# Performance work log

Measured on AMD Instinct MI355X. Metric: run time of the kernel, lower is better.

## Reference

```python
import jax, jax.numpy as jnp
import numpy as np

NUM_BANDS = 64
LATENT = 256
HIDDEN = 512
G = 8
K = 1024
GD = LATENT // G  # 32
BETA = 0.25


def setup_inputs() -> dict:
    key = jax.random.key(0)
    ks = jax.random.split(key, 10)
    B, T = 16, 1000
    bands = jax.random.normal(ks[0], (B, T, NUM_BANDS), dtype=jnp.float32)
    s = 0.02
    enc_w1 = jax.random.normal(ks[1], (NUM_BANDS, HIDDEN), dtype=jnp.float32) * s
    enc_b1 = jnp.zeros((HIDDEN,), dtype=jnp.float32)
    enc_w2 = jax.random.normal(ks[2], (HIDDEN, LATENT), dtype=jnp.float32) * s
    enc_b2 = jnp.zeros((LATENT,), dtype=jnp.float32)
    codebooks = jax.random.normal(ks[3], (G, K, GD), dtype=jnp.float32) * 0.1
    dec_w1 = jax.random.normal(ks[4], (LATENT, HIDDEN), dtype=jnp.float32) * s
    dec_b1 = jnp.zeros((HIDDEN,), dtype=jnp.float32)
    dec_w2 = jax.random.normal(ks[5], (HIDDEN, NUM_BANDS), dtype=jnp.float32) * s
    dec_b2 = jnp.zeros((NUM_BANDS,), dtype=jnp.float32)
    return {
        "bands": bands,
        "enc_w1": enc_w1, "enc_b1": enc_b1, "enc_w2": enc_w2, "enc_b2": enc_b2,
        "codebooks": codebooks,
        "dec_w1": dec_w1, "dec_b1": dec_b1, "dec_w2": dec_w2, "dec_b2": dec_b2,
    }


def _mlp(x, w1, b1, w2, b2):
    # TimeDistributedMLP: Linear -> ReLU -> Linear applied on last dim
    return jax.nn.relu(x @ w1 + b1) @ w2 + b2


def reference(bands, enc_w1, enc_b1, enc_w2, enc_b2, codebooks,
              dec_w1, dec_b1, dec_w2, dec_b2):
    B, T, _ = bands.shape
    z_e = _mlp(bands, enc_w1, enc_b1, enc_w2, enc_b2)  # (B,T,LATENT)

    # Grouped VQ over flattened frames
    parts = z_e.reshape(B * T, G, GD)                   # (N,G,gd)
    zn = jnp.sum(parts * parts, axis=-1)[:, :, None]    # (N,G,1)
    cn = jnp.sum(codebooks * codebooks, axis=-1)[None]  # (1,G,K)
    cross = jnp.einsum('ngd,gkd->ngk', parts, codebooks)
    dist = zn - 2.0 * cross + cn                        # (N,G,K)
    idx = jnp.argmin(dist, axis=-1)                     # (N,G) int
    z_q = codebooks[jnp.arange(G)[None, :], idx]        # (N,G,gd) gather

    # straight-through estimator
    z_q_st = parts + jax.lax.stop_gradient(z_q - parts)

    # per-group mean losses, summed over groups
    codebook_loss = jnp.sum(jnp.mean((jax.lax.stop_gradient(z_q) - parts) ** 2, axis=(0, 2)))
    commit_loss = jnp.sum(jnp.mean((z_q - jax.lax.stop_gradient(parts)) ** 2, axis=(0, 2)))
    vq_loss = BETA * (codebook_loss + commit_loss)  # epoch=None -> beta_eff = beta

    z_q_out = z_q_st.reshape(B, T, LATENT)
    idx_out = idx.reshape(B, T, G)
    bands_hat = _mlp(z_q_out, dec_w1, dec_b1, dec_w2, dec_b2)
    return (bands_hat, z_e, z_q_out, idx_out, vq_loss)
```

## Files before the change

kernel.cpp:

```cpp
#include <hip/hip_runtime.h>

#define NBANDS 64
#define LATENT 256
#define HIDDEN 512
#define GQ 8
#define KQ 1024
#define GD 32
#define NROWS 16000

#define OUT_BH   0
#define OUT_ZE   1024000
#define OUT_ZQ   5120000
#define OUT_IDX  9216000
#define OUT_LOSS 9344000

#define WS_H     0
#define WS_H2BF_F  0
#define WS_ZQB_F   4096000
#define WS_W1B_F   6144000
#define WS_W2B_F   6209536
#define WS_CBH_F   6240000
#define WS_CBM_F   6400000
#define WS_CBL_F   6560000
#define WS_CN    8192000
#define WS_LOSS  8200192

typedef __attribute__((ext_vector_type(8))) short bf16x8;
typedef __attribute__((ext_vector_type(4))) float f32x4;

__device__ __forceinline__ unsigned short f2bf(float f) {
  unsigned u = __builtin_bit_cast(unsigned, f);
  unsigned r = u + 0x7FFFu + ((u >> 16) & 1u);
  return (unsigned short)(r >> 16);
}

__device__ __forceinline__ float bf2f(unsigned short h) {
  return __builtin_bit_cast(float, ((unsigned)h) << 16);
}

__device__ __forceinline__ void split3(float x, unsigned short& h,
                                       unsigned short& m, unsigned short& l) {
  h = f2bf(x);
  const float r1 = x - bf2f(h);
  m = f2bf(r1);
  const float r2 = r1 - bf2f(m);
  l = f2bf(r2);
}

template<int BN, int TM, int TN, int BK, bool RELU>
__global__ __launch_bounds__(256) void gemm_f32(
    const float* __restrict__ A, const float* __restrict__ B,
    const float* __restrict__ bias, float* __restrict__ C,
    int M, int N, int K) {
  constexpr int BM = 128;
  constexpr int NTX = BN / TN;
  constexpr int AF4 = BK / 8;
  constexpr int QPR = BN / 4;
  constexpr int BF4 = BK * BN / 1024;

  __shared__ float As[BK][BM + 8];
  __shared__ float Bs[BK][BN + 4];

  const int tid = threadIdx.x;
  const int tx = tid % NTX;
  const int ty = tid / NTX;
  const int row0 = blockIdx.y * BM;
  const int col0 = blockIdx.x * BN;

  const int arow = tid >> 1;
  const int akq  = (tid & 1) * (BK / 2);

  float acc[TM][TN] = {};

  for (int k0 = 0; k0 < K; k0 += BK) {
    float4 av[AF4], bv[BF4];
#pragma unroll
    for (int q = 0; q < AF4; ++q)
      av[q] = *reinterpret_cast<const float4*>(
          &A[(size_t)(row0 + arow) * K + k0 + akq + q * 4]);
#pragma unroll
    for (int t = 0; t < BF4; ++t) {
      const int qq = tid * BF4 + t;
      const int bk = qq / QPR, bn4 = qq % QPR;
      bv[t] = *reinterpret_cast<const float4*>(
          &B[(size_t)(k0 + bk) * N + col0 + bn4 * 4]);
    }
    __syncthreads();
#pragma unroll
    for (int q = 0; q < AF4; ++q) {
      As[akq + q * 4 + 0][arow] = av[q].x;
      As[akq + q * 4 + 1][arow] = av[q].y;
      As[akq + q * 4 + 2][arow] = av[q].z;
      As[akq + q * 4 + 3][arow] = av[q].w;
    }
#pragma unroll
    for (int t = 0; t < BF4; ++t) {
      const int qq = tid * BF4 + t;
      const int bk = qq / QPR, bn4 = qq % QPR;
      *reinterpret_cast<float4*>(&Bs[bk][bn4 * 4]) = bv[t];
    }
    __syncthreads();

#pragma unroll
    for (int kk = 0; kk < BK; ++kk) {
      float a[TM], b[TN];
#pragma unroll
      for (int q = 0; q < TM / 4; ++q) {
        float4 v = *reinterpret_cast<const float4*>(&As[kk][ty * TM + q * 4]);
        a[q * 4 + 0] = v.x; a[q * 4 + 1] = v.y;
        a[q * 4 + 2] = v.z; a[q * 4 + 3] = v.w;
      }
#pragma unroll
      for (int q = 0; q < TN / 4; ++q) {
        float4 v = *reinterpret_cast<const float4*>(&Bs[kk][tx * TN + q * 4]);
        b[q * 4 + 0] = v.x; b[q * 4 + 1] = v.y;
        b[q * 4 + 2] = v.z; b[q * 4 + 3] = v.w;
      }
#pragma unroll
      for (int i = 0; i < TM; ++i)
#pragma unroll
        for (int j = 0; j < TN; ++j)
          acc[i][j] = fmaf(a[i], b[j], acc[i][j]);
    }
  }

  float bb[TN];
#pragma unroll
  for (int q = 0; q < TN / 4; ++q) {
    float4 v = *reinterpret_cast<const float4*>(&bias[col0 + tx * TN + q * 4]);
    bb[q * 4 + 0] = v.x; bb[q * 4 + 1] = v.y;
    bb[q * 4 + 2] = v.z; bb[q * 4 + 3] = v.w;
  }
#pragma unroll
  for (int i = 0; i < TM; ++i) {
    const int r = row0 + ty * TM + i;
#pragma unroll
    for (int q = 0; q < TN / 4; ++q) {
      float4 v;
      float* vp = &v.x;
#pragma unroll
      for (int j = 0; j < 4; ++j) {
        float t = acc[i][q * 4 + j] + bb[q * 4 + j];
        if (RELU) t = fmaxf(t, 0.0f);
        vp[j] = t;
      }
      *reinterpret_cast<float4*>(&C[(size_t)r * N + col0 + tx * TN + q * 4]) = v;
    }
  }
}

template<int WM, bool OUT_BF16, bool DO_LOSS>
__global__ __launch_bounds__(256) void gemm_bf16_mfma(
    const unsigned short* __restrict__ A, const unsigned short* __restrict__ BT,
    const float* __restrict__ bias, void* __restrict__ Cout,
    int M, int N, int K,
    const float* __restrict__ loss_acc, float* __restrict__ loss_out) {
  constexpr int BM = 4 * WM;
  constexpr int MT = WM / 16;

  __shared__ unsigned short As[BM][40];
  __shared__ unsigned short Bs[64][40];

  const int tid  = threadIdx.x;
  const int wave = tid >> 6;
  const int lane = tid & 63;
  const int quad = lane >> 4;
  const int l16  = lane & 15;
  const int row0 = blockIdx.y * BM;
  const int col0 = blockIdx.x * 64;

  if (DO_LOSS && blockIdx.x == 0 && blockIdx.y == 0 && tid == 0)
    loss_out[0] = 0.5f * loss_acc[0] / (float)((size_t)NROWS * GD);

  f32x4 acc[MT][4];
#pragma unroll
  for (int mt = 0; mt < MT; ++mt)
#pragma unroll
    for (int nt = 0; nt < 4; ++nt) acc[mt][nt] = (f32x4){0.f, 0.f, 0.f, 0.f};

  for (int k0 = 0; k0 < K; k0 += 32) {
    __syncthreads();
    if constexpr (BM == 128) {
      const int r = tid >> 1, seg = (tid & 1) * 16;
      const uint4* src = reinterpret_cast<const uint4*>(
          &A[(size_t)(row0 + r) * K + k0 + seg]);
      uint4* dst = reinterpret_cast<uint4*>(&As[r][seg]);
      dst[0] = src[0]; dst[1] = src[1];
    } else {
      const int r = tid >> 2, seg = (tid & 3) * 8;
      *reinterpret_cast<uint4*>(&As[r][seg]) =
          *reinterpret_cast<const uint4*>(&A[(size_t)(row0 + r) * K + k0 + seg]);
    }
    {
      const int n = tid >> 2, kc = (tid & 3) * 8;
      *reinterpret_cast<uint4*>(&Bs[n][kc]) =
          *reinterpret_cast<const uint4*>(&BT[(size_t)(col0 + n) * K + k0 + kc]);
    }
    __syncthreads();

    bf16x8 af[MT], bf[4];
#pragma unroll
    for (int mt = 0; mt < MT; ++mt)
      af[mt] = *reinterpret_cast<const bf16x8*>(
          &As[wave * WM + mt * 16 + l16][quad * 8]);
#pragma unroll
    for (int nt = 0; nt < 4; ++nt)
      bf[nt] = *reinterpret_cast<const bf16x8*>(&Bs[nt * 16 + l16][quad * 8]);
#pragma unroll
    for (int mt = 0; mt < MT; ++mt)
#pragma unroll
      for (int nt = 0; nt < 4; ++nt)
        acc[mt][nt] = __builtin_amdgcn_mfma_f32_16x16x32_bf16(
            af[mt], bf[nt], acc[mt][nt], 0, 0, 0);
  }

#pragma unroll
  for (int mt = 0; mt < MT; ++mt)
#pragma unroll
    for (int nt = 0; nt < 4; ++nt) {
      const int col = col0 + nt * 16 + l16;
      const float bv = bias[col];
#pragma unroll
      for (int r = 0; r < 4; ++r) {
        const int grow = row0 + wave * WM + mt * 16 + quad * 4 + r;
        float v = acc[mt][nt][r] + bv;
        if constexpr (OUT_BF16) {
          v = fmaxf(v, 0.0f);
          ((unsigned short*)Cout)[(size_t)grow * N + col] = f2bf(v);
        } else {
          ((float*)Cout)[(size_t)grow * N + col] = v;
        }
      }
    }
}

__global__ void prep_cn(const float* __restrict__ cb, float* __restrict__ cn,
                        float* __restrict__ loss_acc) {
  const int i = blockIdx.x * 256 + threadIdx.x;
  if (i == 0) loss_acc[0] = 0.0f;
  if (i < GQ * KQ) {
    const float* c = cb + (size_t)i * GD;
    float s = 0.0f;
#pragma unroll
    for (int d = 0; d < GD; ++d) s = fmaf(c[d], c[d], s);
    cn[i] = -0.5f * s;
  }
}

__global__ void prep_wT(const float* __restrict__ w1, const float* __restrict__ w2,
                        const float* __restrict__ cbk,
                        unsigned short* __restrict__ w1bT,
                        unsigned short* __restrict__ w2bT,
                        unsigned short* __restrict__ cbh,
                        unsigned short* __restrict__ cbm,
                        unsigned short* __restrict__ cbl) {
  const int t = blockIdx.x * 256 + threadIdx.x;
  if (t < 16384) {
    const int n = t >> 5, k0 = (t & 31) * 8;
    alignas(16) unsigned short o[8];
#pragma unroll
    for (int q = 0; q < 8; ++q) o[q] = f2bf(w1[(size_t)(k0 + q) * HIDDEN + n]);
    *reinterpret_cast<uint4*>(&w1bT[(size_t)n * LATENT + k0]) =
        *reinterpret_cast<const uint4*>(o);
  } else if (t < 20480) {
    const int u = t - 16384;
    const int n = u >> 6, k0 = (u & 63) * 8;
    alignas(16) unsigned short o[8];
#pragma unroll
    for (int q = 0; q < 8; ++q) o[q] = f2bf(w2[(size_t)(k0 + q) * NBANDS + n]);
    *reinterpret_cast<uint4*>(&w2bT[(size_t)n * HIDDEN + k0]) =
        *reinterpret_cast<const uint4*>(o);
  } else if (t < 53248) {
    const int e0 = (t - 20480) * 8;
    alignas(16) unsigned short oh[8], om[8], ol[8];
#pragma unroll
    for (int q = 0; q < 8; ++q) split3(cbk[e0 + q], oh[q], om[q], ol[q]);
    *reinterpret_cast<uint4*>(&cbh[e0]) = *reinterpret_cast<const uint4*>(oh);
    *reinterpret_cast<uint4*>(&cbm[e0]) = *reinterpret_cast<const uint4*>(om);
    *reinterpret_cast<uint4*>(&cbl[e0]) = *reinterpret_cast<const uint4*>(ol);
  }
}

struct VqStg { uint4 h, m, l; float c; };

__device__ __forceinline__ void vq_ldg(
    VqStg& s, const unsigned short* __restrict__ cbh,
    const unsigned short* __restrict__ cbm,
    const unsigned short* __restrict__ cbl,
    const float* __restrict__ cng, int gsh, int ch, int tid) {
  const int o = gsh + ch * 2048 + tid * 8;
  s.h = *reinterpret_cast<const uint4*>(&cbh[o]);
  s.m = *reinterpret_cast<const uint4*>(&cbm[o]);
  s.l = *reinterpret_cast<const uint4*>(&cbl[o]);
  if (tid < 64) s.c = cng[ch * 64 + tid];
}

__device__ __forceinline__ void vq_stl(
    unsigned short (&buf)[6272], const VqStg& s, int tid) {
  *reinterpret_cast<uint4*>(&buf[tid * 8])        = s.h;
  *reinterpret_cast<uint4*>(&buf[2048 + tid * 8]) = s.m;
  *reinterpret_cast<uint4*>(&buf[4096 + tid * 8]) = s.l;
  if (tid < 64) *reinterpret_cast<float*>(&buf[6144 + tid * 2]) = s.c;
}

__device__ __forceinline__ void vq_pair(
    const bf16x8 (&ah)[2], const bf16x8 (&am)[2], const bf16x8 (&al)[2],
    const unsigned short (&buf)[6272], int laneoff, int nt0, int ch, int l16,
    float (&best)[8], int (&bidx)[8]) {
  bf16x8 Fh[2], Fm[2], Fl[2];
  float  Fc[2];
#pragma unroll
  for (int p = 0; p < 2; ++p) {
    const int off = laneoff + (nt0 + p) * 512;
    Fh[p] = *reinterpret_cast<const bf16x8*>(&buf[off]);
    Fm[p] = *reinterpret_cast<const bf16x8*>(&buf[2048 + off]);
    Fl[p] = *reinterpret_cast<const bf16x8*>(&buf[4096 + off]);
    Fc[p] = *reinterpret_cast<const float*>(&buf[6144 + (((nt0 + p) * 16 + l16) << 1)]);
  }
  f32x4 a00 = {Fc[0], Fc[0], Fc[0], Fc[0]};
  f32x4 a01 = a00;
  f32x4 a10 = {Fc[1], Fc[1], Fc[1], Fc[1]};
  f32x4 a11 = a10;
  a00 = __builtin_amdgcn_mfma_f32_16x16x32_bf16(ah[0], Fh[0], a00, 0, 0, 0);
  a01 = __builtin_amdgcn_mfma_f32_16x16x32_bf16(ah[1], Fh[0], a01, 0, 0, 0);
  a10 = __builtin_amdgcn_mfma_f32_16x16x32_bf16(ah[0], Fh[1], a10, 0, 0, 0);
  a11 = __builtin_amdgcn_mfma_f32_16x16x32_bf16(ah[1], Fh[1], a11, 0, 0, 0);
  a00 = __builtin_amdgcn_mfma_f32_16x16x32_bf16(ah[0], Fm[0], a00, 0, 0, 0);
  a01 = __builtin_amdgcn_mfma_f32_16x16x32_bf16(ah[1], Fm[0], a01, 0, 0, 0);
  a10 = __builtin_amdgcn_mfma_f32_16x16x32_bf16(ah[0], Fm[1], a10, 0, 0, 0);
  a11 = __builtin_amdgcn_mfma_f32_16x16x32_bf16(ah[1], Fm[1], a11, 0, 0, 0);
  a00 = __builtin_amdgcn_mfma_f32_16x16x32_bf16(am[0], Fh[0], a00, 0, 0, 0);
  a01 = __builtin_amdgcn_mfma_f32_16x16x32_bf16(am[1], Fh[0], a01, 0, 0, 0);
  a10 = __builtin_amdgcn_mfma_f32_16x16x32_bf16(am[0], Fh[1], a10, 0, 0, 0);
  a11 = __builtin_amdgcn_mfma_f32_16x16x32_bf16(am[1], Fh[1], a11, 0, 0, 0);
  a00 = __builtin_amdgcn_mfma_f32_16x16x32_bf16(ah[0], Fl[0], a00, 0, 0, 0);
  a01 = __builtin_amdgcn_mfma_f32_16x16x32_bf16(ah[1], Fl[0], a01, 0, 0, 0);
  a10 = __builtin_amdgcn_mfma_f32_16x16x32_bf16(ah[0], Fl[1], a10, 0, 0, 0);
  a11 = __builtin_amdgcn_mfma_f32_16x16x32_bf16(ah[1], Fl[1], a11, 0, 0, 0);
  a00 = __builtin_amdgcn_mfma_f32_16x16x32_bf16(am[0], Fm[0], a00, 0, 0, 0);
  a01 = __builtin_amdgcn_mfma_f32_16x16x32_bf16(am[1], Fm[0], a01, 0, 0, 0);
  a10 = __builtin_amdgcn_mfma_f32_16x16x32_bf16(am[0], Fm[1], a10, 0, 0, 0);
  a11 = __builtin_amdgcn_mfma_f32_16x16x32_bf16(am[1], Fm[1], a11, 0, 0, 0);
  a00 = __builtin_amdgcn_mfma_f32_16x16x32_bf16(al[0], Fh[0], a00, 0, 0, 0);
  a01 = __builtin_amdgcn_mfma_f32_16x16x32_bf16(al[1], Fh[0], a01, 0, 0, 0);
  a10 = __builtin_amdgcn_mfma_f32_16x16x32_bf16(al[0], Fh[1], a10, 0, 0, 0);
  a11 = __builtin_amdgcn_mfma_f32_16x16x32_bf16(al[1], Fh[1], a11, 0, 0, 0);
  {
    const int code = ch * 64 + nt0 * 16 + l16;
#pragma unroll
    for (int r = 0; r < 4; ++r) {
      if (a00[r] > best[r])     { best[r]     = a00[r]; bidx[r]     = code; }
      if (a01[r] > best[4 + r]) { best[4 + r] = a01[r]; bidx[4 + r] = code; }
    }
  }
  {
    const int code = ch * 64 + (nt0 + 1) * 16 + l16;
#pragma unroll
    for (int r = 0; r < 4; ++r) {
      if (a10[r] > best[r])     { best[r]     = a10[r]; bidx[r]     = code; }
      if (a11[r] > best[4 + r]) { best[4 + r] = a11[r]; bidx[4 + r] = code; }
    }
  }
}

__global__ __launch_bounds__(256, 3) void vq_mfma(
    const float* __restrict__ z_e, const float* __restrict__ cb,
    const float* __restrict__ cnh,
    const unsigned short* __restrict__ cbh,
    const unsigned short* __restrict__ cbm,
    const unsigned short* __restrict__ cbl,
    float* __restrict__ z_q, unsigned short* __restrict__ zqb,
    float* __restrict__ idx_out, float* __restrict__ loss_acc) {
  __shared__ __align__(16) unsigned short lds[2][6272];

  const int g    = blockIdx.y;
  const int row0 = blockIdx.x * 128;
  const int tid  = threadIdx.x;
  const int wave = tid >> 6;
  const int lane = tid & 63;
  const int quad = lane >> 4;
  const int l16  = lane & 15;

  const int gsh = g * (KQ * GD);
  const float* cng = cnh + g * KQ;
  const size_t cb0 = (size_t)g * KQ * GD;
  const int laneoff = l16 * 32 + quad * 8;

  VqStg sX, sY;
  vq_ldg(sX, cbh, cbm, cbl, cng, gsh, 0, tid);

  bf16x8 ah[2], am[2], al[2];
#pragma unroll
  for (int mt = 0; mt < 2; ++mt) {
    const float* zp = &z_e[(size_t)(row0 + wave * 32 + mt * 16 + l16) * LATENT
                           + g * GD + quad * 8];
    const float4 x0 = *reinterpret_cast<const float4*>(zp);
    const float4 x1 = *reinterpret_cast<const float4*>(zp + 4);
    const float xv[8] = {x0.x, x0.y, x0.z, x0.w, x1.x, x1.y, x1.z, x1.w};
    bf16x8 vh, vm, vl;
#pragma unroll
    for (int j = 0; j < 8; ++j) {
      unsigned short sh, sm, sl;
      split3(xv[j], sh, sm, sl);
      vh[j] = (short)sh; vm[j] = (short)sm; vl[j] = (short)sl;
    }
    ah[mt] = vh; am[mt] = vm; al[mt] = vl;
  }

  float best[8];
  int   bidx[8];
#pragma unroll
  for (int i = 0; i < 8; ++i) { best[i] = -3.0e38f; bidx[i] = 0; }

  vq_stl(lds[0], sX, tid);
  vq_ldg(sY, cbh, cbm, cbl, cng, gsh, 1, tid);
  __syncthreads();

#pragma unroll 1
  for (int cp = 0; cp < 8; ++cp) {
    const int ch = 2 * cp;
    if (ch < 14) vq_ldg(sX, cbh, cbm, cbl, cng, gsh, ch + 2, tid);
    vq_pair(ah, am, al, lds[0], laneoff, 0, ch, l16, best, bidx);
    vq_pair(ah, am, al, lds[0], laneoff, 2, ch, l16, best, bidx);
    vq_stl(lds[1], sY, tid);
    __syncthreads();

    const int ch2 = ch + 1;
    if (ch2 < 14) vq_ldg(sY, cbh, cbm, cbl, cng, gsh, ch2 + 2, tid);
    vq_pair(ah, am, al, lds[1], laneoff, 0, ch2, l16, best, bidx);
    vq_pair(ah, am, al, lds[1], laneoff, 2, ch2, l16, best, bidx);
    if (ch2 < 15) {
      vq_stl(lds[0], sX, tid);
      __syncthreads();
    }
  }

  float sse_local = 0.0f;
#pragma unroll
  for (int s8 = 0; s8 < 8; ++s8) {
    float mb = best[s8];
    int   mi = bidx[s8];
#pragma unroll
    for (int m = 1; m < 16; m <<= 1) {
      const float ov = __shfl_xor(mb, m, 64);
      const int   oi = __shfl_xor(mi, m, 64);
      if (ov > mb || (ov == mb && oi < mi)) { mb = ov; mi = oi; }
    }
    const int mt  = s8 >> 2;
    const int r   = s8 & 3;
    const int row = row0 + wave * 32 + mt * 16 + quad * 4 + r;
    const float2 cw = *reinterpret_cast<const float2*>(
        &cb[cb0 + (size_t)mi * GD + 2 * l16]);
    const float2 zv = *reinterpret_cast<const float2*>(
        &z_e[(size_t)row * LATENT + g * GD + 2 * l16]);
    const float d0 = cw.x - zv.x;
    const float d1 = cw.y - zv.y;
    sse_local = fmaf(d0, d0, fmaf(d1, d1, sse_local));
    *reinterpret_cast<float2*>(
        &z_q[(size_t)row * LATENT + g * GD + 2 * l16]) = cw;
    const unsigned pz = (unsigned)f2bf(cw.x) | ((unsigned)f2bf(cw.y) << 16);
    *reinterpret_cast<unsigned*>(
        &zqb[(size_t)row * LATENT + g * GD + 2 * l16]) = pz;
    if (l16 == 0) idx_out[(size_t)row * GQ + g] = (float)mi;
  }

#pragma unroll
  for (int m = 1; m < 64; m <<= 1) sse_local += __shfl_xor(sse_local, m, 64);
  if (lane == 0) atomicAdd(loss_acc, sse_local);
}

extern "C" void kernel_launch(void* const* d_in, const int* in_sizes, int n_in,
                              void* d_out, int out_size, void* d_ws, size_t ws_size,
                              hipStream_t stream) {
  const float* bands  = (const float*)d_in[0];
  const float* enc_w1 = (const float*)d_in[1];
  const float* enc_b1 = (const float*)d_in[2];
  const float* enc_w2 = (const float*)d_in[3];
  const float* enc_b2 = (const float*)d_in[4];
  const float* cbooks = (const float*)d_in[5];
  const float* dec_w1 = (const float*)d_in[6];
  const float* dec_b1 = (const float*)d_in[7];
  const float* dec_w2 = (const float*)d_in[8];
  const float* dec_b2 = (const float*)d_in[9];

  float* out = (float*)d_out;
  float* ws  = (float*)d_ws;

  float* bands_hat = out + OUT_BH;
  float* z_e       = out + OUT_ZE;
  float* z_q       = out + OUT_ZQ;
  float* idx_f     = out + OUT_IDX;
  float* loss_out  = out + OUT_LOSS;

  float* H        = ws + WS_H;
  float* cn       = ws + WS_CN;
  float* loss_acc = ws + WS_LOSS;
  unsigned short* h2bf = (unsigned short*)(ws + WS_H2BF_F);
  unsigned short* zqb  = (unsigned short*)(ws + WS_ZQB_F);
  unsigned short* w1bT = (unsigned short*)(ws + WS_W1B_F);
  unsigned short* w2bT = (unsigned short*)(ws + WS_W2B_F);
  unsigned short* cbh  = (unsigned short*)(ws + WS_CBH_F);
  unsigned short* cbm  = (unsigned short*)(ws + WS_CBM_F);
  unsigned short* cbl  = (unsigned short*)(ws + WS_CBL_F);

  prep_cn<<<dim3(32), dim3(256), 0, stream>>>(cbooks, cn, loss_acc);

  gemm_f32<128, 8, 8, 16, true ><<<dim3(HIDDEN / 128, NROWS / 128), dim3(256), 0, stream>>>(
      bands, enc_w1, enc_b1, H, NROWS, HIDDEN, NBANDS);
  gemm_f32<64, 4, 8, 32, false><<<dim3(LATENT / 64, NROWS / 128), dim3(256), 0, stream>>>(
      H, enc_w2, enc_b2, z_e, NROWS, LATENT, HIDDEN);

  prep_wT<<<dim3(208), dim3(256), 0, stream>>>(
      dec_w1, dec_w2, cbooks, w1bT, w2bT, cbh, cbm, cbl);

  vq_mfma<<<dim3(NROWS / 128, GQ), dim3(256), 0, stream>>>(
      z_e, cbooks, cn, cbh, cbm, cbl, z_q, zqb, idx_f, loss_acc);

  gemm_bf16_mfma<32, true, true ><<<dim3(HIDDEN / 64, NROWS / 128), dim3(256), 0, stream>>>(
      zqb, w1bT, dec_b1, (void*)h2bf, NROWS, HIDDEN, LATENT, loss_acc, loss_out);
  gemm_bf16_mfma<16, false, false><<<dim3(NBANDS / 64, NROWS / 64), dim3(256), 0, stream>>>(
      h2bf, w2bT, dec_b2, (void*)bands_hat, NROWS, NBANDS, HIDDEN, loss_acc, loss_out);
}
```

Measured before the change: 320.0 us.

## Pre-swizzle codebook chunks into LDS-ready records and halve VQ staging registers

The prep kernel now writes the hi/mid/lo bf16 codebook splits and the norm terms into per-chunk records already laid out in MFMA fragment order. The VQ kernel can then copy each record into LDS contiguously and read fragments with lane-linear offsets, which should avoid strided LDS reads and bank conflicts. Staging uses one register set instead of two, and launch bounds are raised to 4 blocks per CU to reduce register pressure and raise occupancy. In exchange the prep kernel does a scattered write pattern and runs more threads to copy the norms into the records.

```diff
diff --git a/kernel.cpp b/kernel.cpp
--- a/kernel.cpp
+++ b/kernel.cpp
@@ -19,9 +19,8 @@
 #define WS_ZQB_F   4096000
 #define WS_W1B_F   6144000
 #define WS_W2B_F   6209536
-#define WS_CBH_F   6240000
-#define WS_CBM_F   6400000
-#define WS_CBL_F   6560000
+#define WS_REC_F   6240000
+#define VQ_REC_SH  6272
 #define WS_CN    8192000
 #define WS_LOSS  8200192
 
@@ -248,12 +247,10 @@
 }
 
 __global__ void prep_wT(const float* __restrict__ w1, const float* __restrict__ w2,
-                        const float* __restrict__ cbk,
+                        const float* __restrict__ cbk, const float* __restrict__ cn,
                         unsigned short* __restrict__ w1bT,
                         unsigned short* __restrict__ w2bT,
-                        unsigned short* __restrict__ cbh,
-                        unsigned short* __restrict__ cbm,
-                        unsigned short* __restrict__ cbl) {
+                        unsigned short* __restrict__ rec) {
   const int t = blockIdx.x * 256 + threadIdx.x;
   if (t < 16384) {
     const int n = t >> 5, k0 = (t & 31) * 8;
@@ -272,46 +269,53 @@
         *reinterpret_cast<const uint4*>(o);
   } else if (t < 53248) {
     const int e0 = (t - 20480) * 8;
+    const int gidx = e0 >> 15;
+    const int w    = e0 & 32767;
+    const int code = w >> 5;
+    const int d0   = w & 31;
+    const int quad = d0 >> 3;
+    const int ch   = code >> 6;
+    const int cw   = code & 63;
+    const int nt   = cw >> 4;
+    const int l16  = cw & 15;
+    const int slot = nt * 64 + quad * 16 + l16;
+    unsigned short* recb = rec + (size_t)(gidx * 16 + ch) * VQ_REC_SH;
     alignas(16) unsigned short oh[8], om[8], ol[8];
 #pragma unroll
     for (int q = 0; q < 8; ++q) split3(cbk[e0 + q], oh[q], om[q], ol[q]);
-    *reinterpret_cast<uint4*>(&cbh[e0]) = *reinterpret_cast<const uint4*>(oh);
-    *reinterpret_cast<uint4*>(&cbm[e0]) = *reinterpret_cast<const uint4*>(om);
-    *reinterpret_cast<uint4*>(&cbl[e0]) = *reinterpret_cast<const uint4*>(ol);
-  }
-}
-
-struct VqStg { uint4 h, m, l; float c; };
-
-__device__ __forceinline__ void vq_ldg(
-    VqStg& s, const unsigned short* __restrict__ cbh,
-    const unsigned short* __restrict__ cbm,
-    const unsigned short* __restrict__ cbl,
-    const float* __restrict__ cng, int gsh, int ch, int tid) {
-  const int o = gsh + ch * 2048 + tid * 8;
-  s.h = *reinterpret_cast<const uint4*>(&cbh[o]);
-  s.m = *reinterpret_cast<const uint4*>(&cbm[o]);
-  s.l = *reinterpret_cast<const uint4*>(&cbl[o]);
-  if (tid < 64) s.c = cng[ch * 64 + tid];
-}
-
-__device__ __forceinline__ void vq_stl(
-    unsigned short (&buf)[6272], const VqStg& s, int tid) {
-  *reinterpret_cast<uint4*>(&buf[tid * 8])        = s.h;
-  *reinterpret_cast<uint4*>(&buf[2048 + tid * 8]) = s.m;
-  *reinterpret_cast<uint4*>(&buf[4096 + tid * 8]) = s.l;
-  if (tid < 64) *reinterpret_cast<float*>(&buf[6144 + tid * 2]) = s.c;
+    *reinterpret_cast<uint4*>(&recb[slot * 8]) =
+        *reinterpret_cast<const uint4*>(oh);
+    *reinterpret_cast<uint4*>(&recb[2048 + slot * 8]) =
+        *reinterpret_cast<const uint4*>(om);
+    *reinterpret_cast<uint4*>(&recb[4096 + slot * 8]) =
+        *reinterpret_cast<const uint4*>(ol);
+  } else if (t < 61440) {
+    const int i = t - 53248;
+    const int gidx = i >> 10, code = i & 1023;
+    const int ch = code >> 6, cw = code & 63;
+    unsigned short* recb = rec + (size_t)(gidx * 16 + ch) * VQ_REC_SH;
+    *reinterpret_cast<float*>(&recb[6144 + cw * 2]) = cn[(size_t)gidx * KQ + code];
+  }
+}
+
+__device__ __forceinline__ void vq_write(
+    unsigned short (&buf)[VQ_REC_SH], int tid,
+    const uint4& h, const uint4& m, const uint4& l, float c) {
+  *reinterpret_cast<uint4*>(&buf[tid * 8])        = h;
+  *reinterpret_cast<uint4*>(&buf[2048 + tid * 8]) = m;
+  *reinterpret_cast<uint4*>(&buf[4096 + tid * 8]) = l;
+  if (tid < 64) *reinterpret_cast<float*>(&buf[6144 + tid * 2]) = c;
 }
 
 __device__ __forceinline__ void vq_pair(
     const bf16x8 (&ah)[2], const bf16x8 (&am)[2], const bf16x8 (&al)[2],
-    const unsigned short (&buf)[6272], int laneoff, int nt0, int ch, int l16,
+    const unsigned short (&buf)[VQ_REC_SH], int lane, int l16, int nt0, int ch,
     float (&best)[8], int (&bidx)[8]) {
   bf16x8 Fh[2], Fm[2], Fl[2];
   float  Fc[2];
 #pragma unroll
   for (int p = 0; p < 2; ++p) {
-    const int off = laneoff + (nt0 + p) * 512;
+    const int off = ((nt0 + p) * 64 + lane) * 8;
     Fh[p] = *reinterpret_cast<const bf16x8*>(&buf[off]);
     Fm[p] = *reinterpret_cast<const bf16x8*>(&buf[2048 + off]);
     Fl[p] = *reinterpret_cast<const bf16x8*>(&buf[4096 + off]);
@@ -363,15 +367,13 @@
   }
 }
 
-__global__ __launch_bounds__(256, 3) void vq_mfma(
+__global__ __launch_bounds__(256, 4) void vq_mfma(
     const float* __restrict__ z_e, const float* __restrict__ cb,
-    const float* __restrict__ cnh,
-    const unsigned short* __restrict__ cbh,
-    const unsigned short* __restrict__ cbm,
-    const unsigned short* __restrict__ cbl,
+    const unsigned short* __restrict__ rec,
     float* __restrict__ z_q, unsigned short* __restrict__ zqb,
     float* __restrict__ idx_out, float* __restrict__ loss_acc) {
-  __shared__ __align__(16) unsigned short lds[2][6272];
+  __shared__ __align__(16) unsigned short lds0[VQ_REC_SH];
+  __shared__ __align__(16) unsigned short lds1[VQ_REC_SH];
 
   const int g    = blockIdx.y;
   const int row0 = blockIdx.x * 128;
@@ -381,13 +383,19 @@
   const int quad = lane >> 4;
   const int l16  = lane & 15;
 
-  const int gsh = g * (KQ * GD);
-  const float* cng = cnh + g * KQ;
+  const unsigned short* recg = rec + (size_t)g * 16 * VQ_REC_SH;
   const size_t cb0 = (size_t)g * KQ * GD;
-  const int laneoff = l16 * 32 + quad * 8;
-
-  VqStg sX, sY;
-  vq_ldg(sX, cbh, cbm, cbl, cng, gsh, 0, tid);
+
+  uint4 Lh, Lm, Ll; float Lc;
+#define VQ_LDG(chk) do {                                                    \
+    const unsigned short* _b = recg + (chk) * VQ_REC_SH;                    \
+    Lh = *reinterpret_cast<const uint4*>(&_b[tid * 8]);                     \
+    Lm = *reinterpret_cast<const uint4*>(&_b[2048 + tid * 8]);              \
+    Ll = *reinterpret_cast<const uint4*>(&_b[4096 + tid * 8]);              \
+    Lc = *reinterpret_cast<const float*>(&_b[6144 + tid * 2]);              \
+  } while (0)
+
+  VQ_LDG(0);
 
   bf16x8 ah[2], am[2], al[2];
 #pragma unroll
@@ -412,28 +420,28 @@
 #pragma unroll
   for (int i = 0; i < 8; ++i) { best[i] = -3.0e38f; bidx[i] = 0; }
 
-  vq_stl(lds[0], sX, tid);
-  vq_ldg(sY, cbh, cbm, cbl, cng, gsh, 1, tid);
+  vq_write(lds0, tid, Lh, Lm, Ll, Lc);
+  VQ_LDG(1);
   __syncthreads();
 
 #pragma unroll 1
   for (int cp = 0; cp < 8; ++cp) {
-    const int ch = 2 * cp;
-    if (ch < 14) vq_ldg(sX, cbh, cbm, cbl, cng, gsh, ch + 2, tid);
-    vq_pair(ah, am, al, lds[0], laneoff, 0, ch, l16, best, bidx);
-    vq_pair(ah, am, al, lds[0], laneoff, 2, ch, l16, best, bidx);
-    vq_stl(lds[1], sY, tid);
+    const int c = 2 * cp;
+    vq_pair(ah, am, al, lds0, lane, l16, 0, c, best, bidx);
+    vq_pair(ah, am, al, lds0, lane, l16, 2, c, best, bidx);
+    vq_write(lds1, tid, Lh, Lm, Ll, Lc);
+    if (c + 2 < 16) VQ_LDG(c + 2);
     __syncthreads();
 
-    const int ch2 = ch + 1;
-    if (ch2 < 14) vq_ldg(sY, cbh, cbm, cbl, cng, gsh, ch2 + 2, tid);
-    vq_pair(ah, am, al, lds[1], laneoff, 0, ch2, l16, best, bidx);
-    vq_pair(ah, am, al, lds[1], laneoff, 2, ch2, l16, best, bidx);
-    if (ch2 < 15) {
-      vq_stl(lds[0], sX, tid);
+    vq_pair(ah, am, al, lds1, lane, l16, 0, c + 1, best, bidx);
+    vq_pair(ah, am, al, lds1, lane, l16, 2, c + 1, best, bidx);
+    if (c + 2 < 16) {
+      vq_write(lds0, tid, Lh, Lm, Ll, Lc);
+      if (c + 3 < 16) VQ_LDG(c + 3);
       __syncthreads();
     }
   }
+#undef VQ_LDG
 
   float sse_local = 0.0f;
 #pragma unroll
@@ -499,9 +507,7 @@
   unsigned short* zqb  = (unsigned short*)(ws + WS_ZQB_F);
   unsigned short* w1bT = (unsigned short*)(ws + WS_W1B_F);
   unsigned short* w2bT = (unsigned short*)(ws + WS_W2B_F);
-  unsigned short* cbh  = (unsigned short*)(ws + WS_CBH_F);
-  unsigned short* cbm  = (unsigned short*)(ws + WS_CBM_F);
-  unsigned short* cbl  = (unsigned short*)(ws + WS_CBL_F);
+  unsigned short* rec  = (unsigned short*)(ws + WS_REC_F);
 
   prep_cn<<<dim3(32), dim3(256), 0, stream>>>(cbooks, cn, loss_acc);
 
@@ -510,11 +516,11 @@
   gemm_f32<64, 4, 8, 32, false><<<dim3(LATENT / 64, NROWS / 128), dim3(256), 0, stream>>>(
       H, enc_w2, enc_b2, z_e, NROWS, LATENT, HIDDEN);
 
-  prep_wT<<<dim3(208), dim3(256), 0, stream>>>(
-      dec_w1, dec_w2, cbooks, w1bT, w2bT, cbh, cbm, cbl);
+  prep_wT<<<dim3(240), dim3(256), 0, stream>>>(
+      dec_w1, dec_w2, cbooks, cn, w1bT, w2bT, rec);
 
   vq_mfma<<<dim3(NROWS / 128, GQ), dim3(256), 0, stream>>>(
-      z_e, cbooks, cn, cbh, cbm, cbl, z_q, zqb, idx_f, loss_acc);
+      z_e, cbooks, rec, z_q, zqb, idx_f, loss_acc);
 
   gemm_bf16_mfma<32, true, true ><<<dim3(HIDDEN / 64, NROWS / 128), dim3(256), 0, stream>>>(
       zqb, w1bT, dec_b1, (void*)h2bf, NROWS, HIDDEN, LATENT, loss_acc, loss_out);
```

Result: slower. 327.0 us (+2.2%).
